# Kernel optimization log

Measured on AMD Instinct MI355X. Metric: run time of the kernel, lower is better.

Reference implementation:

```python
import jax, jax.numpy as jnp
import numpy as np

B, N, OUT = 32, 2048, 100

def setup_inputs() -> dict:
    key = jax.random.key(0)
    k1, k2 = jax.random.split(key)
    query = jax.random.normal(k1, (B, N), dtype=jnp.float32) * 10.0
    # Dense(100, use_bias=False) kernel, glorot-ish scale
    W = jax.random.normal(k2, (N, OUT), dtype=jnp.float32) * (1.0 / np.sqrt(N))
    return {"query": query, "W": W}

def reference(query, W):
    # Faithful translation of the TF graph:
    # cast -> expand_dims(1)/(2) -> broadcast add -> cast -> reduce_sum(axis=1)
    c = query.astype(jnp.int32)                      # [B, N]
    g = c[:, None, :] + c[:, :, None]                # [B, N, N], g[b,i,j] = c[b,j] + c[b,i]
    f = g.astype(jnp.float32)
    f_reduced = jnp.sum(f, axis=1)                   # [B, N] == N*c[b,j] + sum_i c[b,i]
    diff = query - f_reduced
    rem = diff * diff                                # squared diff
    return rem @ W                                   # [B, 100]
```

## Files before the change

kernel.cpp:

```cpp
#include <hip/hip_runtime.h>

#define BATCH  32
#define NDIM   2048
#define NOUT   100
#define SPLIT  16
#define SLICE  (NDIM / SPLIT)
#define BLOCK  256

__global__ __launch_bounds__(BLOCK)
void fused_model_kernel(const float* __restrict__ q,
                        const float* __restrict__ W,
                        float* __restrict__ out)
{
    const int s = blockIdx.x;
    const int b = blockIdx.y;
    const int t = threadIdx.x;

    __shared__ float rem_lds[SLICE];
    __shared__ int   wave_sum[BLOCK / 64];
    __shared__ float half_partial[128];
    __shared__ int   S_lds;

    const float* qrow = q + b * NDIM;

    int csum = 0;
    #pragma unroll
    for (int k = 0; k < NDIM / BLOCK; ++k)
        csum += (int)qrow[k * BLOCK + t];

    #pragma unroll
    for (int m = 32; m > 0; m >>= 1)
        csum += __shfl_xor(csum, m, 64);
    if ((t & 63) == 0) wave_sum[t >> 6] = csum;
    __syncthreads();
    if (t == 0) {
        int ssum = 0;
        #pragma unroll
        for (int w = 0; w < BLOCK / 64; ++w) ssum += wave_sum[w];
        S_lds = ssum;
    }
    __syncthreads();
    const int S = S_lds;

    if (t < SLICE) {
        float v = qrow[s * SLICE + t];
        int   c = (int)v;
        float d = v - (float)(NDIM * c + S);
        rem_lds[t] = d * d;
    }
    __syncthreads();

    const int o = t & 127;
    const int h = t >> 7;
    float acc = 0.f;
    if (o < NOUT) {
        const int jbeg = h * (SLICE / 2);
        const float* Wbase = W + (size_t)(s * SLICE + jbeg) * NOUT + o;
        #pragma unroll 8
        for (int j = 0; j < SLICE / 2; ++j) {
            acc += rem_lds[jbeg + j] * Wbase[(size_t)j * NOUT];
        }
    }
    if (h == 1 && o < NOUT) half_partial[o] = acc;
    __syncthreads();
    if (h == 0 && o < NOUT) {
        acc += half_partial[o];
        atomicAdd(&out[b * NOUT + o], acc);
    }
}

extern "C" void kernel_launch(void* const* d_in, const int* in_sizes, int n_in,
                              void* d_out, int out_size, void* d_ws, size_t ws_size,
                              hipStream_t stream) {
    const float* q = (const float*)d_in[0];
    const float* W = (const float*)d_in[1];
    float* out = (float*)d_out;

    hipMemsetAsync(out, 0, (size_t)out_size * sizeof(float), stream);

    dim3 grid(SPLIT, BATCH);
    fused_model_kernel<<<grid, BLOCK, 0, stream>>>(q, W, out);
}
```

Before: 60.03 us.

## Partition work by output-column groups instead of K-slices, drop atomics and memset

The grid now splits over groups of 8 output columns per batch row instead of 16 K-slices. Each block computes the full 2048-element rem vector in LDS from float4 loads and reduces across 32 K-chunks with shuffles plus a small LDS step. Because each block owns its outputs, the atomicAdd and the separate hipMemsetAsync launch go away. In exchange, every block recomputes the whole rem row, and each thread reads only 8 contiguous W floats per row, which gives narrower memory access than the earlier 100-column coalesced rows.

```diff
diff --git a/kernel.cpp b/kernel.cpp
--- a/kernel.cpp
+++ b/kernel.cpp
@@ -3,69 +3,80 @@
 #define BATCH  32
 #define NDIM   2048
 #define NOUT   100
-#define SPLIT  16
-#define SLICE  (NDIM / SPLIT)
+#define OG     8
+#define NOG    13
 #define BLOCK  256
+#define NCHUNK (BLOCK / OG)
+#define CHUNK  (NDIM / NCHUNK)
 
 __global__ __launch_bounds__(BLOCK)
 void fused_model_kernel(const float* __restrict__ q,
                         const float* __restrict__ W,
                         float* __restrict__ out)
 {
-    const int s = blockIdx.x;
+    const int g = blockIdx.x;
     const int b = blockIdx.y;
     const int t = threadIdx.x;
 
-    __shared__ float rem_lds[SLICE];
+    __shared__ float rem_lds[NDIM];
     __shared__ int   wave_sum[BLOCK / 64];
-    __shared__ float half_partial[128];
+    __shared__ float wred[BLOCK / 64][OG];
     __shared__ int   S_lds;
 
-    const float* qrow = q + b * NDIM;
+    const float4* qrow4 = (const float4*)(q + b * NDIM);
+    const float4 v0 = qrow4[t];
+    const float4 v1 = qrow4[BLOCK + t];
 
-    int csum = 0;
-    #pragma unroll
-    for (int k = 0; k < NDIM / BLOCK; ++k)
-        csum += (int)qrow[k * BLOCK + t];
+    const int c0x = (int)v0.x, c0y = (int)v0.y, c0z = (int)v0.z, c0w = (int)v0.w;
+    const int c1x = (int)v1.x, c1y = (int)v1.y, c1z = (int)v1.z, c1w = (int)v1.w;
+    int csum = c0x + c0y + c0z + c0w + c1x + c1y + c1z + c1w;
 
     #pragma unroll
-    for (int m = 32; m > 0; m >>= 1)
-        csum += __shfl_xor(csum, m, 64);
+    for (int m = 32; m > 0; m >>= 1) csum += __shfl_xor(csum, m, 64);
     if ((t & 63) == 0) wave_sum[t >> 6] = csum;
     __syncthreads();
-    if (t == 0) {
-        int ssum = 0;
-        #pragma unroll
-        for (int w = 0; w < BLOCK / 64; ++w) ssum += wave_sum[w];
-        S_lds = ssum;
-    }
+    if (t == 0)
+        S_lds = wave_sum[0] + wave_sum[1] + wave_sum[2] + wave_sum[3];
     __syncthreads();
     const int S = S_lds;
 
-    if (t < SLICE) {
-        float v = qrow[s * SLICE + t];
-        int   c = (int)v;
-        float d = v - (float)(NDIM * c + S);
-        rem_lds[t] = d * d;
+    {
+        const int j0 = 4 * t, j1 = 4 * BLOCK + 4 * t;
+        float d;
+        d = v0.x - (float)(NDIM * c0x + S); rem_lds[j0 + 0] = d * d;
+        d = v0.y - (float)(NDIM * c0y + S); rem_lds[j0 + 1] = d * d;
+        d = v0.z - (float)(NDIM * c0z + S); rem_lds[j0 + 2] = d * d;
+        d = v0.w - (float)(NDIM * c0w + S); rem_lds[j0 + 3] = d * d;
+        d = v1.x - (float)(NDIM * c1x + S); rem_lds[j1 + 0] = d * d;
+        d = v1.y - (float)(NDIM * c1y + S); rem_lds[j1 + 1] = d * d;
+        d = v1.z - (float)(NDIM * c1z + S); rem_lds[j1 + 2] = d * d;
+        d = v1.w - (float)(NDIM * c1w + S); rem_lds[j1 + 3] = d * d;
     }
     __syncthreads();
 
-    const int o = t & 127;
-    const int h = t >> 7;
+    const int o    = t & (OG - 1);
+    const int ch   = t >> 3;
+    const int ocol = g * OG + o;
+    const int jb   = ch * CHUNK;
+
     float acc = 0.f;
-    if (o < NOUT) {
-        const int jbeg = h * (SLICE / 2);
-        const float* Wbase = W + (size_t)(s * SLICE + jbeg) * NOUT + o;
+    if (ocol < NOUT) {
+        const float* Wb = W + (size_t)jb * NOUT + ocol;
         #pragma unroll 8
-        for (int j = 0; j < SLICE / 2; ++j) {
-            acc += rem_lds[jbeg + j] * Wbase[(size_t)j * NOUT];
-        }
+        for (int j = 0; j < CHUNK; ++j)
+            acc += rem_lds[jb + j] * Wb[(size_t)j * NOUT];
     }
-    if (h == 1 && o < NOUT) half_partial[o] = acc;
+
+    acc += __shfl_xor(acc, 8, 64);
+    acc += __shfl_xor(acc, 16, 64);
+    acc += __shfl_xor(acc, 32, 64);
+    if ((t & 63) < OG) wred[t >> 6][o] = acc;
     __syncthreads();
-    if (h == 0 && o < NOUT) {
-        acc += half_partial[o];
-        atomicAdd(&out[b * NOUT + o], acc);
+
+    if (t < OG) {
+        const int oc = g * OG + t;
+        if (oc < NOUT)
+            out[b * NOUT + oc] = wred[0][t] + wred[1][t] + wred[2][t] + wred[3][t];
     }
 }
 
@@ -76,8 +87,6 @@
     const float* W = (const float*)d_in[1];
     float* out = (float*)d_out;
 
-    hipMemsetAsync(out, 0, (size_t)out_size * sizeof(float), stream);
-
-    dim3 grid(SPLIT, BATCH);
+    dim3 grid(NOG, BATCH);
     fused_model_kernel<<<grid, BLOCK, 0, stream>>>(q, W, out);
 }
```

Result: no change. 59.77 us (-0.4%).
